# Performance work log

Measured on AMD Instinct MI355X. Metric: run time of the kernel, lower is better.

## Reference

```python
import jax, jax.numpy as jnp
import numpy as np

CHUNK = 64  # rows of `a` processed per step to bound the [chunk, N, d] abs-diff intermediate
TAIL_K = 4          # selection_tail_size
FAR_K = 64          # far_sample_count
PUSH_K = 4          # pushing_sample_size
HUBER_DELTA = 1.0   # torch.nn.HuberLoss default


def cdist_l1(a, b):
    # a: [M, d], b: [N, d] -> [M, N] Manhattan distances, computed in row chunks
    M, d = a.shape
    def f(a_chunk):  # [CHUNK, d] -> [CHUNK, N]
        return jnp.abs(a_chunk[:, None, :] - b[None, :, :]).sum(-1)
    return jax.lax.map(f, a.reshape(-1, CHUNK, d)).reshape(M, b.shape[0])


def smallest_k_mean(dists, k):
    # mean of the k smallest entries along last dim
    neg_vals, _ = jax.lax.top_k(-dists, k)
    return (-neg_vals).mean(-1)


def huber(x):
    # HuberLoss(pred=x, target=0), delta=1
    ax = jnp.abs(x)
    return jnp.where(ax < HUBER_DELTA, 0.5 * x * x, HUBER_DELTA * (ax - 0.5 * HUBER_DELTA))


def setup_inputs() -> dict:
    key = jax.random.key(0)
    k1, k2 = jax.random.split(key)
    space_samples = jax.random.normal(k1, (2048, 256), dtype=jnp.float32)
    latents = jax.random.normal(k2, (8192, 256), dtype=jnp.float32)
    return {"space_samples": space_samples, "latents": latents}


def reference(space_samples, latents):
    # space_samples: [M, d] drawn from latent_sampler; latents: [N, d]
    space_dists = cdist_l1(space_samples, latents)            # [M, N]
    tail_dists = smallest_k_mean(space_dists, TAIL_K)          # [M]
    far_inds = jax.lax.top_k(tail_dists, FAR_K)[1]             # [FAR_K]
    far_samples = space_samples[far_inds]                      # [FAR_K, d]
    empty_dists = cdist_l1(far_samples, latents)               # [FAR_K, N]
    close_dists = smallest_k_mean(empty_dists, PUSH_K)         # [FAR_K]
    return huber(close_dists).mean()
```

## Files before the change

### kernel.cpp

```cpp
#include <hip/hip_runtime.h>
#include <hip/hip_bf16.h>


static constexpr int M = 2048;
static constexpr int N = 8192;
static constexpr int KQ = 64;
static constexpr int BKQ = 16;
static constexpr int ROWS_PER_BLK = 128;
static constexpr int COLS_PER_BLK = 128;
static constexpr int NCHUNK = N / COLS_PER_BLK;
static constexpr int SLD_RED = 68;

static constexpr float QS  = 21.0f;
static constexpr float QB  = 126.0f;
static constexpr float INV_QS = 1.0f / 21.0f;

__device__ __forceinline__ float med3f(float a, float b, float c) {
    return __builtin_amdgcn_fmed3f(a, b, c);
}

__device__ __forceinline__ void ins4(float d, float& s0, float& s1, float& s2, float& s3) {
    float n0 = fminf(s0, d);
    float n1 = med3f(s0, s1, d);
    float n2 = med3f(s1, s2, d);
    float n3 = med3f(s2, s3, d);
    s0 = n0; s1 = n1; s2 = n2; s3 = n3;
}

__device__ __forceinline__ unsigned int sad8(unsigned int a, unsigned int b, unsigned int c) {
#if __has_builtin(__builtin_amdgcn_sad_u8)
    return __builtin_amdgcn_sad_u8(a, b, c);
#else
    unsigned int d;
    asm("v_sad_u8 %0, %1, %2, %3" : "=v"(d) : "v"(a), "v"(b), "v"(c));
    return d;
#endif
}

__device__ __forceinline__ unsigned int quant4(const float4 v) {
    const float y0 = fminf(fmaxf(fmaf(v.x, QS, QB), 0.0f), 255.0f);
    const float y1 = fminf(fmaxf(fmaf(v.y, QS, QB), 0.0f), 255.0f);
    const float y2 = fminf(fmaxf(fmaf(v.z, QS, QB), 0.0f), 255.0f);
    const float y3 = fminf(fmaxf(fmaf(v.w, QS, QB), 0.0f), 255.0f);
    const unsigned int b0 = (unsigned int)(int)rintf(y0);
    const unsigned int b1 = (unsigned int)(int)rintf(y1);
    const unsigned int b2 = (unsigned int)(int)rintf(y2);
    const unsigned int b3 = (unsigned int)(int)rintf(y3);
    return b0 | (b1 << 8) | (b2 << 16) | (b3 << 24);
}

__device__ __forceinline__ float huber_pos(float x) {
    const float ax = __builtin_fabsf(x);
    return (ax < 1.0f) ? (0.5f * x * x) : (ax - 0.5f);
}

__global__ __launch_bounds__(256)
void convert_kernel(const float* __restrict__ A, const float* __restrict__ B,
                    unsigned int* __restrict__ At, unsigned int* __restrict__ Bt) {
    __shared__ unsigned int lt[KQ * 65];
    const int tid = threadIdx.x;
    const bool isB = (blockIdx.x < N / 64);
    const float* src = isB ? B : A;
    unsigned int* dst = isB ? Bt : At;
    const int rows = isB ? N : M;
    const int r0 = (isB ? blockIdx.x : (blockIdx.x - N / 64)) * 64;

#pragma unroll
    for (int it = 0; it < 16; ++it) {
        const int qi = it * 256 + tid;
        const int row = qi >> 6;
        const int kq = qi & 63;
        const float4 v = *(const float4*)&src[(r0 + row) * 256 + 4 * kq];
        lt[kq * 65 + row] = quant4(v);
    }
    __syncthreads();
#pragma unroll
    for (int it = 0; it < 16; ++it) {
        const int wi = it * 256 + tid;
        const int row = wi & 63;
        const int kq = wi >> 6;
        dst[(size_t)kq * rows + r0 + row] = lt[kq * 65 + row];
    }
}

__global__ __launch_bounds__(256, 4)
void dist4_kernel(const unsigned int* __restrict__ At, const unsigned int* __restrict__ Bt,
                  float4* __restrict__ ws_dist) {
    __shared__ __align__(16) char smem[34816];
    unsigned int* tiles = (unsigned int*)smem;
    const int tid = threadIdx.x;
    const int tx = tid & 15;
    const int ty = tid >> 4;
    const int bx = blockIdx.x;
    const int by = blockIdx.y;
    const int rowBase = by * ROWS_PER_BLK;
    const int colBase = bx * COLS_PER_BLK;

    const int sKq = tid >> 5;
    const int sC  = (tid & 31) * 4;

    unsigned int acc[8][8];
#pragma unroll
    for (int i = 0; i < 8; ++i)
#pragma unroll
        for (int j = 0; j < 8; ++j) acc[i][j] = 0u;

    uint4 pa0, pa1, pb0, pb1;
    pa0 = *(const uint4*)&At[(sKq) * M + rowBase + sC];
    pa1 = *(const uint4*)&At[(sKq + 8) * M + rowBase + sC];
    pb0 = *(const uint4*)&Bt[(sKq) * N + colBase + sC];
    pb1 = *(const uint4*)&Bt[(sKq + 8) * N + colBase + sC];
    {
        unsigned int* As = tiles;
        unsigned int* Bs = tiles + 2048;
        *(uint4*)&As[sKq * 128 + sC] = pa0;
        *(uint4*)&As[(sKq + 8) * 128 + sC] = pa1;
        *(uint4*)&Bs[sKq * 128 + sC] = pb0;
        *(uint4*)&Bs[(sKq + 8) * 128 + sC] = pb1;
    }

    for (int t0 = 0; t0 < KQ / BKQ; ++t0) {
        __syncthreads();
        if (t0 + 1 < KQ / BKQ) {
            const int kb = (t0 + 1) * BKQ;
            pa0 = *(const uint4*)&At[(kb + sKq) * M + rowBase + sC];
            pa1 = *(const uint4*)&At[(kb + sKq + 8) * M + rowBase + sC];
            pb0 = *(const uint4*)&Bt[(kb + sKq) * N + colBase + sC];
            pb1 = *(const uint4*)&Bt[(kb + sKq + 8) * N + colBase + sC];
        }

        const unsigned int* As = tiles + (t0 & 1) * 4096;
        const unsigned int* Bs = As + 2048;
#pragma unroll 4
        for (int kq = 0; kq < BKQ; ++kq) {
            const uint4 aw0 = *(const uint4*)&As[kq * 128 + 8 * ty];
            const uint4 aw1 = *(const uint4*)&As[kq * 128 + 8 * ty + 4];
            const uint4 bw0 = *(const uint4*)&Bs[kq * 128 + 4 * tx];
            const uint4 bw1 = *(const uint4*)&Bs[kq * 128 + 64 + 4 * tx];
            const unsigned int a[8] = {aw0.x, aw0.y, aw0.z, aw0.w, aw1.x, aw1.y, aw1.z, aw1.w};
            const unsigned int b[8] = {bw0.x, bw0.y, bw0.z, bw0.w, bw1.x, bw1.y, bw1.z, bw1.w};
#pragma unroll
            for (int i = 0; i < 8; ++i) {
#pragma unroll
                for (int j = 0; j < 8; ++j) {
                    acc[i][j] = sad8(a[i], b[j], acc[i][j]);
                }
            }
        }

        if (t0 + 1 < KQ / BKQ) {
            __syncthreads();
            unsigned int* Asw = tiles + ((t0 + 1) & 1) * 4096;
            unsigned int* Bsw = Asw + 2048;
            *(uint4*)&Asw[sKq * 128 + sC] = pa0;
            *(uint4*)&Asw[(sKq + 8) * 128 + sC] = pa1;
            *(uint4*)&Bsw[sKq * 128 + sC] = pb0;
            *(uint4*)&Bsw[(sKq + 8) * 128 + sC] = pb1;
        }
    }

    float s[8][4];
#pragma unroll
    for (int i = 0; i < 8; ++i) {
        float s0 = 1e30f, s1 = 1e30f, s2 = 1e30f, s3 = 1e30f;
#pragma unroll
        for (int j = 0; j < 8; ++j) {
            const float d = (float)acc[i][j] * INV_QS;
            ins4(d, s0, s1, s2, s3);
        }
        s[i][0] = s0; s[i][1] = s1; s[i][2] = s2; s[i][3] = s3;
    }

    __syncthreads();
    float (*red)[SLD_RED] = (float (*)[SLD_RED])smem;
#pragma unroll
    for (int i = 0; i < 8; ++i) {
        *(float4*)&red[8 * ty + i][4 * tx] = make_float4(s[i][0], s[i][1], s[i][2], s[i][3]);
    }
    __syncthreads();

    if (tid < ROWS_PER_BLK) {
        float s0 = 1e30f, s1 = 1e30f, s2 = 1e30f, s3 = 1e30f;
#pragma unroll
        for (int c = 0; c < 16; ++c) {
            const float4 v = *(const float4*)&red[tid][4 * c];
            ins4(v.x, s0, s1, s2, s3);
            ins4(v.y, s0, s1, s2, s3);
            ins4(v.z, s0, s1, s2, s3);
            ins4(v.w, s0, s1, s2, s3);
        }
        ws_dist[bx * M + rowBase + tid] = make_float4(s0, s1, s2, s3);
    }
}

__global__ __launch_bounds__(256)
void tail_kernel(const float4* __restrict__ ws_dist, float* __restrict__ tail) {
    const int gtid = blockIdx.x * 256 + threadIdx.x;
    const int row = gtid >> 3;
    const int q = gtid & 7;
    float s0 = 1e30f, s1 = 1e30f, s2 = 1e30f, s3 = 1e30f;
#pragma unroll
    for (int c = 0; c < 8; ++c) {
        const float4 v = ws_dist[(q * 8 + c) * M + row];
        ins4(v.x, s0, s1, s2, s3);
        ins4(v.y, s0, s1, s2, s3);
        ins4(v.z, s0, s1, s2, s3);
        ins4(v.w, s0, s1, s2, s3);
    }
#pragma unroll
    for (int lvl = 1; lvl <= 4; lvl <<= 1) {
        const float o0 = __shfl_xor(s0, lvl, 64);
        const float o1 = __shfl_xor(s1, lvl, 64);
        const float o2 = __shfl_xor(s2, lvl, 64);
        const float o3 = __shfl_xor(s3, lvl, 64);
        ins4(o0, s0, s1, s2, s3);
        ins4(o1, s0, s1, s2, s3);
        ins4(o2, s0, s1, s2, s3);
        ins4(o3, s0, s1, s2, s3);
    }
    if (q == 0) tail[row] = (s0 + s1 + s2 + s3) * 0.25f;
}

__global__ __launch_bounds__(1024)
void top64_kernel(const float* __restrict__ tail, float* __restrict__ out) {
    __shared__ unsigned int hist[8][256];
    __shared__ unsigned int ctrl[2];
    __shared__ float wsum[16];
    __shared__ unsigned int wcnt[16];
    const int tid = threadIdx.x;
    const int wid = tid >> 6;
    const int lane = tid & 63;

    const unsigned int k0 = __float_as_uint(tail[tid]);
    const unsigned int k1 = __float_as_uint(tail[tid + 1024]);

    if (tid == 0) { ctrl[0] = 0u; ctrl[1] = 64u; }

    for (int p = 0; p < 4; ++p) {
        const int shift = 24 - 8 * p;
        ((unsigned int*)hist)[tid] = 0u;
        ((unsigned int*)hist)[tid + 1024] = 0u;
        __syncthreads();
        const unsigned int prefix = ctrl[0];
        const unsigned int t = ctrl[1];
        bool c0 = true, c1 = true;
        if (p > 0) {
            const int sh8 = shift + 8;
            c0 = ((k0 >> sh8) == (prefix >> sh8));
            c1 = ((k1 >> sh8) == (prefix >> sh8));
        }
        if (c0) atomicAdd(&hist[wid & 7][(k0 >> shift) & 255], 1u);
        if (c1) atomicAdd(&hist[wid & 7][(k1 >> shift) & 255], 1u);
        __syncthreads();
        if (tid < 256) {
            unsigned int h = 0;
#pragma unroll
            for (int r = 0; r < 8; ++r) h += hist[r][tid];
            hist[0][tid] = h;
        }
        __syncthreads();
        if (wid == 0) {
            const unsigned int s4 = hist[0][4 * lane] + hist[0][4 * lane + 1] +
                                    hist[0][4 * lane + 2] + hist[0][4 * lane + 3];
            unsigned int suf = s4;
#pragma unroll
            for (int off = 1; off < 64; off <<= 1) {
                const unsigned int v = __shfl_down(suf, off, 64);
                if (lane + off < 64) suf += v;
            }
            const unsigned long long mask = __ballot(suf >= t);
            const int lstar = 63 - __clzll(mask);
            if (lane == lstar) {
                unsigned int c = suf - s4;
                for (int d = 4 * lstar + 3; d >= 4 * lstar; --d) {
                    const unsigned int cd = hist[0][d];
                    c += cd;
                    if (c >= t) {
                        ctrl[0] = prefix | ((unsigned int)d << shift);
                        ctrl[1] = t - (c - cd);
                        break;
                    }
                }
            }
        }
        __syncthreads();
    }

    const unsigned int T = ctrl[0];
    float sum = 0.0f;
    unsigned int cnt = 0;
    if (k0 > T) { ++cnt; sum += huber_pos(__uint_as_float(k0)); }
    if (k1 > T) { ++cnt; sum += huber_pos(__uint_as_float(k1)); }
#pragma unroll
    for (int off = 32; off > 0; off >>= 1) {
        sum += __shfl_down(sum, off, 64);
        cnt += __shfl_down(cnt, off, 64);
    }
    if (lane == 0) { wsum[wid] = sum; wcnt[wid] = cnt; }
    __syncthreads();
    if (tid == 0) {
        float S = 0.0f;
        unsigned int C = 0;
#pragma unroll
        for (int w = 0; w < 16; ++w) { S += wsum[w]; C += wcnt[w]; }
        const float hT = huber_pos(__uint_as_float(T));
        out[0] = (S + (float)(64u - C) * hT) * (1.0f / 64.0f);
    }
}

extern "C" void kernel_launch(void* const* d_in, const int* in_sizes, int n_in,
                              void* d_out, int out_size, void* d_ws, size_t ws_size,
                              hipStream_t stream) {
    const float* A = (const float*)d_in[0];
    const float* B = (const float*)d_in[1];
    float* out = (float*)d_out;

    unsigned int* Bt = (unsigned int*)d_ws;
    unsigned int* At = (unsigned int*)((char*)d_ws + (size_t)KQ * N * 4);
    float4* ws_dist = (float4*)((char*)d_ws + (size_t)KQ * N * 4 + (size_t)KQ * M * 4);
    float* tail = (float*)((char*)ws_dist + (size_t)NCHUNK * M * sizeof(float4));

    convert_kernel<<<dim3(N / 64 + M / 64), 256, 0, stream>>>(A, B, At, Bt);
    dist4_kernel<<<dim3(NCHUNK, M / ROWS_PER_BLK), 256, 0, stream>>>(At, Bt, ws_dist);
    tail_kernel<<<dim3(M * 8 / 256), 256, 0, stream>>>(ws_dist, tail);
    top64_kernel<<<1, 1024, 0, stream>>>(tail, out);
}
```

Before: 112.1 us.

## Enlarge distance kernel tile to 256 rows with 16x8 per-thread accumulators

Doubles the rows handled per block in the quantized SAD distance kernel, so each thread accumulates a 16x8 register tile instead of 8x8. This halves the B-tile global and LDS traffic per computed distance and raises arithmetic intensity per LDS load. The cost is higher register use and shared memory, so occupancy drops to 2 blocks per CU, and the final top-4 reduction runs in two passes through the shared buffer. The grid also has half as many blocks, which risks leaving CUs idle.

```diff
diff --git a/kernel.cpp b/kernel.cpp
--- a/kernel.cpp
+++ b/kernel.cpp
@@ -6,7 +6,7 @@
 static constexpr int N = 8192;
 static constexpr int KQ = 64;
 static constexpr int BKQ = 16;
-static constexpr int ROWS_PER_BLK = 128;
+static constexpr int ROWS_PER_BLK = 256;
 static constexpr int COLS_PER_BLK = 128;
 static constexpr int NCHUNK = N / COLS_PER_BLK;
 static constexpr int SLD_RED = 68;
@@ -83,10 +83,10 @@
     }
 }
 
-__global__ __launch_bounds__(256, 4)
+__global__ __launch_bounds__(256, 2)
 void dist4_kernel(const unsigned int* __restrict__ At, const unsigned int* __restrict__ Bt,
                   float4* __restrict__ ws_dist) {
-    __shared__ __align__(16) char smem[34816];
+    __shared__ __align__(16) char smem[49152];
     unsigned int* tiles = (unsigned int*)smem;
     const int tid = threadIdx.x;
     const int tx = tid & 15;
@@ -96,51 +96,65 @@
     const int rowBase = by * ROWS_PER_BLK;
     const int colBase = bx * COLS_PER_BLK;
 
-    const int sKq = tid >> 5;
-    const int sC  = (tid & 31) * 4;
-
-    unsigned int acc[8][8];
-#pragma unroll
-    for (int i = 0; i < 8; ++i)
+    const int aKq = tid >> 6;
+    const int aC  = (tid & 63) * 4;
+    const int bKq = tid >> 5;
+    const int bC  = (tid & 31) * 4;
+
+    unsigned int acc[16][8];
+#pragma unroll
+    for (int i = 0; i < 16; ++i)
 #pragma unroll
         for (int j = 0; j < 8; ++j) acc[i][j] = 0u;
 
-    uint4 pa0, pa1, pb0, pb1;
-    pa0 = *(const uint4*)&At[(sKq) * M + rowBase + sC];
-    pa1 = *(const uint4*)&At[(sKq + 8) * M + rowBase + sC];
-    pb0 = *(const uint4*)&Bt[(sKq) * N + colBase + sC];
-    pb1 = *(const uint4*)&Bt[(sKq + 8) * N + colBase + sC];
+    uint4 pa0, pa1, pa2, pa3, pb0, pb1;
+    pa0 = *(const uint4*)&At[(aKq     ) * M + rowBase + aC];
+    pa1 = *(const uint4*)&At[(aKq +  4) * M + rowBase + aC];
+    pa2 = *(const uint4*)&At[(aKq +  8) * M + rowBase + aC];
+    pa3 = *(const uint4*)&At[(aKq + 12) * M + rowBase + aC];
+    pb0 = *(const uint4*)&Bt[(bKq     ) * N + colBase + bC];
+    pb1 = *(const uint4*)&Bt[(bKq +  8) * N + colBase + bC];
     {
         unsigned int* As = tiles;
-        unsigned int* Bs = tiles + 2048;
-        *(uint4*)&As[sKq * 128 + sC] = pa0;
-        *(uint4*)&As[(sKq + 8) * 128 + sC] = pa1;
-        *(uint4*)&Bs[sKq * 128 + sC] = pb0;
-        *(uint4*)&Bs[(sKq + 8) * 128 + sC] = pb1;
+        unsigned int* Bs = tiles + 4096;
+        *(uint4*)&As[(aKq     ) * 256 + aC] = pa0;
+        *(uint4*)&As[(aKq +  4) * 256 + aC] = pa1;
+        *(uint4*)&As[(aKq +  8) * 256 + aC] = pa2;
+        *(uint4*)&As[(aKq + 12) * 256 + aC] = pa3;
+        *(uint4*)&Bs[(bKq     ) * 128 + bC] = pb0;
+        *(uint4*)&Bs[(bKq +  8) * 128 + bC] = pb1;
     }
 
     for (int t0 = 0; t0 < KQ / BKQ; ++t0) {
         __syncthreads();
         if (t0 + 1 < KQ / BKQ) {
             const int kb = (t0 + 1) * BKQ;
-            pa0 = *(const uint4*)&At[(kb + sKq) * M + rowBase + sC];
-            pa1 = *(const uint4*)&At[(kb + sKq + 8) * M + rowBase + sC];
-            pb0 = *(const uint4*)&Bt[(kb + sKq) * N + colBase + sC];
-            pb1 = *(const uint4*)&Bt[(kb + sKq + 8) * N + colBase + sC];
-        }
-
-        const unsigned int* As = tiles + (t0 & 1) * 4096;
-        const unsigned int* Bs = As + 2048;
-#pragma unroll 4
+            pa0 = *(const uint4*)&At[(kb + aKq     ) * M + rowBase + aC];
+            pa1 = *(const uint4*)&At[(kb + aKq +  4) * M + rowBase + aC];
+            pa2 = *(const uint4*)&At[(kb + aKq +  8) * M + rowBase + aC];
+            pa3 = *(const uint4*)&At[(kb + aKq + 12) * M + rowBase + aC];
+            pb0 = *(const uint4*)&Bt[(kb + bKq     ) * N + colBase + bC];
+            pb1 = *(const uint4*)&Bt[(kb + bKq +  8) * N + colBase + bC];
+        }
+
+        const unsigned int* As = tiles + (t0 & 1) * 6144;
+        const unsigned int* Bs = As + 4096;
+#pragma unroll 2
         for (int kq = 0; kq < BKQ; ++kq) {
-            const uint4 aw0 = *(const uint4*)&As[kq * 128 + 8 * ty];
-            const uint4 aw1 = *(const uint4*)&As[kq * 128 + 8 * ty + 4];
+            const uint4 aw0 = *(const uint4*)&As[kq * 256 + 16 * ty];
+            const uint4 aw1 = *(const uint4*)&As[kq * 256 + 16 * ty + 4];
+            const uint4 aw2 = *(const uint4*)&As[kq * 256 + 16 * ty + 8];
+            const uint4 aw3 = *(const uint4*)&As[kq * 256 + 16 * ty + 12];
             const uint4 bw0 = *(const uint4*)&Bs[kq * 128 + 4 * tx];
             const uint4 bw1 = *(const uint4*)&Bs[kq * 128 + 64 + 4 * tx];
-            const unsigned int a[8] = {aw0.x, aw0.y, aw0.z, aw0.w, aw1.x, aw1.y, aw1.z, aw1.w};
-            const unsigned int b[8] = {bw0.x, bw0.y, bw0.z, bw0.w, bw1.x, bw1.y, bw1.z, bw1.w};
-#pragma unroll
-            for (int i = 0; i < 8; ++i) {
+            const unsigned int a[16] = {aw0.x, aw0.y, aw0.z, aw0.w,
+                                        aw1.x, aw1.y, aw1.z, aw1.w,
+                                        aw2.x, aw2.y, aw2.z, aw2.w,
+                                        aw3.x, aw3.y, aw3.z, aw3.w};
+            const unsigned int b[8] = {bw0.x, bw0.y, bw0.z, bw0.w,
+                                       bw1.x, bw1.y, bw1.z, bw1.w};
+#pragma unroll
+            for (int i = 0; i < 16; ++i) {
 #pragma unroll
                 for (int j = 0; j < 8; ++j) {
                     acc[i][j] = sad8(a[i], b[j], acc[i][j]);
@@ -150,18 +164,20 @@
 
         if (t0 + 1 < KQ / BKQ) {
             __syncthreads();
-            unsigned int* Asw = tiles + ((t0 + 1) & 1) * 4096;
-            unsigned int* Bsw = Asw + 2048;
-            *(uint4*)&Asw[sKq * 128 + sC] = pa0;
-            *(uint4*)&Asw[(sKq + 8) * 128 + sC] = pa1;
-            *(uint4*)&Bsw[sKq * 128 + sC] = pb0;
-            *(uint4*)&Bsw[(sKq + 8) * 128 + sC] = pb1;
-        }
-    }
-
-    float s[8][4];
-#pragma unroll
-    for (int i = 0; i < 8; ++i) {
+            unsigned int* Asw = tiles + ((t0 + 1) & 1) * 6144;
+            unsigned int* Bsw = Asw + 4096;
+            *(uint4*)&Asw[(aKq     ) * 256 + aC] = pa0;
+            *(uint4*)&Asw[(aKq +  4) * 256 + aC] = pa1;
+            *(uint4*)&Asw[(aKq +  8) * 256 + aC] = pa2;
+            *(uint4*)&Asw[(aKq + 12) * 256 + aC] = pa3;
+            *(uint4*)&Bsw[(bKq     ) * 128 + bC] = pb0;
+            *(uint4*)&Bsw[(bKq +  8) * 128 + bC] = pb1;
+        }
+    }
+
+    float s[16][4];
+#pragma unroll
+    for (int i = 0; i < 16; ++i) {
         float s0 = 1e30f, s1 = 1e30f, s2 = 1e30f, s3 = 1e30f;
 #pragma unroll
         for (int j = 0; j < 8; ++j) {
@@ -171,25 +187,30 @@
         s[i][0] = s0; s[i][1] = s1; s[i][2] = s2; s[i][3] = s3;
     }
 
-    __syncthreads();
     float (*red)[SLD_RED] = (float (*)[SLD_RED])smem;
 #pragma unroll
-    for (int i = 0; i < 8; ++i) {
-        *(float4*)&red[8 * ty + i][4 * tx] = make_float4(s[i][0], s[i][1], s[i][2], s[i][3]);
-    }
-    __syncthreads();
-
-    if (tid < ROWS_PER_BLK) {
-        float s0 = 1e30f, s1 = 1e30f, s2 = 1e30f, s3 = 1e30f;
-#pragma unroll
-        for (int c = 0; c < 16; ++c) {
-            const float4 v = *(const float4*)&red[tid][4 * c];
-            ins4(v.x, s0, s1, s2, s3);
-            ins4(v.y, s0, s1, s2, s3);
-            ins4(v.z, s0, s1, s2, s3);
-            ins4(v.w, s0, s1, s2, s3);
-        }
-        ws_dist[bx * M + rowBase + tid] = make_float4(s0, s1, s2, s3);
+    for (int p = 0; p < 2; ++p) {
+        __syncthreads();
+        if ((ty >> 3) == p) {
+#pragma unroll
+            for (int i = 0; i < 16; ++i) {
+                *(float4*)&red[16 * (ty & 7) + i][4 * tx] =
+                    make_float4(s[i][0], s[i][1], s[i][2], s[i][3]);
+            }
+        }
+        __syncthreads();
+        if (tid < 128) {
+            float s0 = 1e30f, s1 = 1e30f, s2 = 1e30f, s3 = 1e30f;
+#pragma unroll
+            for (int c = 0; c < 16; ++c) {
+                const float4 v = *(const float4*)&red[tid][4 * c];
+                ins4(v.x, s0, s1, s2, s3);
+                ins4(v.y, s0, s1, s2, s3);
+                ins4(v.z, s0, s1, s2, s3);
+                ins4(v.w, s0, s1, s2, s3);
+            }
+            ws_dist[bx * M + rowBase + p * 128 + tid] = make_float4(s0, s1, s2, s3);
+        }
     }
 }
 
```

Measured after the change: 113.6 us. Within noise of the previous version (+1.3%).

## Use triple-buffered LDS tiles with smaller K step and one barrier per step

Applied to the files above, without the earlier changes.

Halves the K-step depth to 8 and rotates among three shared-memory buffers, so each step needs only one __syncthreads instead of two. The next tile's shared-memory store is issued between the two halves of the compute loop to overlap it with SAD work. The inner loop is fully unrolled. This doubles the number of steps and barriers per tile pass and changes LDS footprint and register pressure.

```diff
diff --git a/kernel.cpp b/kernel.cpp
--- a/kernel.cpp
+++ b/kernel.cpp
@@ -5,11 +5,13 @@
 static constexpr int M = 2048;
 static constexpr int N = 8192;
 static constexpr int KQ = 64;
-static constexpr int BKQ = 16;
+static constexpr int BKQ = 8;
+static constexpr int NSTEP = KQ / BKQ;
 static constexpr int ROWS_PER_BLK = 128;
 static constexpr int COLS_PER_BLK = 128;
 static constexpr int NCHUNK = N / COLS_PER_BLK;
 static constexpr int SLD_RED = 68;
+static constexpr int BUFU = 2048;
 
 static constexpr float QS  = 21.0f;
 static constexpr float QB  = 126.0f;
@@ -105,58 +107,62 @@
 #pragma unroll
         for (int j = 0; j < 8; ++j) acc[i][j] = 0u;
 
-    uint4 pa0, pa1, pb0, pb1;
-    pa0 = *(const uint4*)&At[(sKq) * M + rowBase + sC];
-    pa1 = *(const uint4*)&At[(sKq + 8) * M + rowBase + sC];
-    pb0 = *(const uint4*)&Bt[(sKq) * N + colBase + sC];
-    pb1 = *(const uint4*)&Bt[(sKq + 8) * N + colBase + sC];
     {
-        unsigned int* As = tiles;
-        unsigned int* Bs = tiles + 2048;
-        *(uint4*)&As[sKq * 128 + sC] = pa0;
-        *(uint4*)&As[(sKq + 8) * 128 + sC] = pa1;
-        *(uint4*)&Bs[sKq * 128 + sC] = pb0;
-        *(uint4*)&Bs[(sKq + 8) * 128 + sC] = pb1;
-    }
-
-    for (int t0 = 0; t0 < KQ / BKQ; ++t0) {
-        __syncthreads();
-        if (t0 + 1 < KQ / BKQ) {
+        const uint4 pa = *(const uint4*)&At[sKq * M + rowBase + sC];
+        const uint4 pb = *(const uint4*)&Bt[sKq * N + colBase + sC];
+        *(uint4*)&tiles[sKq * 128 + sC] = pa;
+        *(uint4*)&tiles[1024 + sKq * 128 + sC] = pb;
+    }
+
+    int rb = 0;
+    int wb = BUFU;
+    for (int t0 = 0; t0 < NSTEP; ++t0) {
+        __syncthreads();
+        uint4 pa, pb;
+        const bool pf = (t0 + 1 < NSTEP);
+        if (pf) {
             const int kb = (t0 + 1) * BKQ;
-            pa0 = *(const uint4*)&At[(kb + sKq) * M + rowBase + sC];
-            pa1 = *(const uint4*)&At[(kb + sKq + 8) * M + rowBase + sC];
-            pb0 = *(const uint4*)&Bt[(kb + sKq) * N + colBase + sC];
-            pb1 = *(const uint4*)&Bt[(kb + sKq + 8) * N + colBase + sC];
-        }
-
-        const unsigned int* As = tiles + (t0 & 1) * 4096;
-        const unsigned int* Bs = As + 2048;
-#pragma unroll 4
-        for (int kq = 0; kq < BKQ; ++kq) {
-            const uint4 aw0 = *(const uint4*)&As[kq * 128 + 8 * ty];
-            const uint4 aw1 = *(const uint4*)&As[kq * 128 + 8 * ty + 4];
-            const uint4 bw0 = *(const uint4*)&Bs[kq * 128 + 4 * tx];
-            const uint4 bw1 = *(const uint4*)&Bs[kq * 128 + 64 + 4 * tx];
+            pa = *(const uint4*)&At[(kb + sKq) * M + rowBase + sC];
+            pb = *(const uint4*)&Bt[(kb + sKq) * N + colBase + sC];
+        }
+
+#pragma unroll
+        for (int kq = 0; kq < 4; ++kq) {
+            const uint4 aw0 = *(const uint4*)&tiles[rb + kq * 128 + 8 * ty];
+            const uint4 aw1 = *(const uint4*)&tiles[rb + kq * 128 + 8 * ty + 4];
+            const uint4 bw0 = *(const uint4*)&tiles[rb + 1024 + kq * 128 + 4 * tx];
+            const uint4 bw1 = *(const uint4*)&tiles[rb + 1024 + kq * 128 + 64 + 4 * tx];
             const unsigned int a[8] = {aw0.x, aw0.y, aw0.z, aw0.w, aw1.x, aw1.y, aw1.z, aw1.w};
             const unsigned int b[8] = {bw0.x, bw0.y, bw0.z, bw0.w, bw1.x, bw1.y, bw1.z, bw1.w};
 #pragma unroll
-            for (int i = 0; i < 8; ++i) {
-#pragma unroll
-                for (int j = 0; j < 8; ++j) {
+            for (int i = 0; i < 8; ++i)
+#pragma unroll
+                for (int j = 0; j < 8; ++j)
                     acc[i][j] = sad8(a[i], b[j], acc[i][j]);
-                }
-            }
-        }
-
-        if (t0 + 1 < KQ / BKQ) {
-            __syncthreads();
-            unsigned int* Asw = tiles + ((t0 + 1) & 1) * 4096;
-            unsigned int* Bsw = Asw + 2048;
-            *(uint4*)&Asw[sKq * 128 + sC] = pa0;
-            *(uint4*)&Asw[(sKq + 8) * 128 + sC] = pa1;
-            *(uint4*)&Bsw[sKq * 128 + sC] = pb0;
-            *(uint4*)&Bsw[(sKq + 8) * 128 + sC] = pb1;
-        }
+        }
+
+        if (pf) {
+            *(uint4*)&tiles[wb + sKq * 128 + sC] = pa;
+            *(uint4*)&tiles[wb + 1024 + sKq * 128 + sC] = pb;
+        }
+
+#pragma unroll
+        for (int kq = 4; kq < 8; ++kq) {
+            const uint4 aw0 = *(const uint4*)&tiles[rb + kq * 128 + 8 * ty];
+            const uint4 aw1 = *(const uint4*)&tiles[rb + kq * 128 + 8 * ty + 4];
+            const uint4 bw0 = *(const uint4*)&tiles[rb + 1024 + kq * 128 + 4 * tx];
+            const uint4 bw1 = *(const uint4*)&tiles[rb + 1024 + kq * 128 + 64 + 4 * tx];
+            const unsigned int a[8] = {aw0.x, aw0.y, aw0.z, aw0.w, aw1.x, aw1.y, aw1.z, aw1.w};
+            const unsigned int b[8] = {bw0.x, bw0.y, bw0.z, bw0.w, bw1.x, bw1.y, bw1.z, bw1.w};
+#pragma unroll
+            for (int i = 0; i < 8; ++i)
+#pragma unroll
+                for (int j = 0; j < 8; ++j)
+                    acc[i][j] = sad8(a[i], b[j], acc[i][j]);
+        }
+
+        rb = (rb == 2 * BUFU) ? 0 : rb + BUFU;
+        wb = (wb == 2 * BUFU) ? 0 : wb + BUFU;
     }
 
     float s[8][4];
```

Result: slower. 127.3 us (+13.5%).
